# Optimization experiments

Measured on AMD Instinct MI355X. Metric: run time of the kernel, lower is better.

The kernel has to match this reference:

```python
import jax, jax.numpy as jnp
import numpy as np

B, NIMG, NTXT, EMB, INCH = 16, 1024, 512, 768, 768
EPS = 1e-5


def _bn(x, g, b):
    # train-mode BatchNorm1d over (batch, length) per channel; x: [B, L, C]
    mu = x.mean(axis=(0, 1))
    var = ((x - mu) ** 2).mean(axis=(0, 1))  # biased variance, as torch BN
    return g * (x - mu) * jax.lax.rsqrt(var + EPS) + b


def setup_inputs() -> dict:
    key = jax.random.key(0)
    ks = jax.random.split(key, 5)
    s = 1.0 / np.sqrt(EMB)
    return {
        "image": jax.random.normal(ks[0], (B, NIMG, INCH), jnp.float32),
        "text": jax.random.normal(ks[1], (B, NTXT, EMB), jnp.float32),
        "k": jax.random.uniform(ks[2], (B,), jnp.float32),
        "Wc": jax.random.normal(ks[3], (INCH, EMB), jnp.float32) * s,   # Conv1d k=1 weight
        "bc": jnp.zeros((INCH,), jnp.float32),
        "g1": jnp.ones((INCH,), jnp.float32),
        "b1": jnp.zeros((INCH,), jnp.float32),
        "Wout": jax.random.normal(ks[4], (INCH, EMB), jnp.float32) * s,  # Linear weight
        "bout": jnp.zeros((INCH,), jnp.float32),
        "g2": jnp.ones((INCH,), jnp.float32),
        "b2": jnp.zeros((INCH,), jnp.float32),
    }


def reference(image, text, k, Wc, bc, g1, b1, Wout, bout, g2, b2):
    Bn, N, C = image.shape
    T = text.shape[1]
    # emb1: Conv1d(1x1) -> BN -> ReLU, applied along tokens
    text_emb = jax.nn.relu(_bn(text @ Wc.T + bc, g1, b1))            # [B, T, C]
    attn = jnp.einsum('bnc,btc->bnt', image, text_emb) / np.sqrt(C)  # [B, N, T]
    # per-sample neighbor counts K_neigs = round(N * k)
    K_neigs = jnp.round(N * k).astype(jnp.int32)                     # [B]
    max_k = max(int(np.asarray(jnp.max(K_neigs))), 1)
    # top-k along the image-token axis (dim 1) => top_k on last axis of [B,T,N]
    attn_t = jnp.swapaxes(attn, 1, 2)                                # [B, T, N]
    _, idx = jax.lax.top_k(attn_t, max_k)                            # [B, T, max_k]
    valid = jnp.arange(max_k)[None, None, :] < K_neigs[:, None, None]
    valid = jnp.broadcast_to(valid, idx.shape)                       # [B, T, max_k]
    bi = jnp.arange(Bn)[:, None, None]
    ti = jnp.arange(T)[None, :, None]
    full_mask = jnp.zeros((Bn, T, N), bool).at[bi, ti, idx].set(valid)
    full_mask = jnp.swapaxes(full_mask, 1, 2)                        # [B, N, T]
    attn_sm = jax.nn.softmax(attn, axis=1)                           # softmax over N (dim=-2)
    v = text @ Wout.T + bout                                         # [B, T, C]
    out = jnp.einsum('bnt,btc->bnc', attn_sm * full_mask, v)         # [B, N, C]
    return jax.nn.relu(_bn(out, g2, b2)) + image
```

## Files before the change

kernel.cpp:

```cpp
#include <hip/hip_runtime.h>
#include <hip/hip_bf16.h>
#include <math.h>

typedef __attribute__((ext_vector_type(8))) short short8;
typedef __attribute__((ext_vector_type(4))) float f32x4;

static constexpr int kB  = 16;
static constexpr int kN  = 1024;
static constexpr int kT  = 512;
static constexpr int kC  = 768;
static constexpr float kEps = 1e-5f;

__device__ inline unsigned short f2bf(float x) {
    unsigned u = __float_as_uint(x);
    u += 0x7FFFu + ((u >> 16) & 1u);
    return (unsigned short)(u >> 16);
}
__device__ inline float bf2f(unsigned short h) {
    return __uint_as_float(((unsigned)h) << 16);
}

template<bool HAS_BIAS>
__global__ __launch_bounds__(256)
void gemm_sb(const unsigned short* __restrict__ A, const unsigned short* __restrict__ B,
             float* __restrict__ C, const float* __restrict__ bias,
             int N, int Kseg, float alpha, long sA, long sB, long sC)
{
    __shared__ unsigned short Ah[128 * 32];
    __shared__ unsigned short Al[128 * 32];
    __shared__ unsigned short Bh[128 * 32];
    __shared__ unsigned short Bl[128 * 32];
    const int bz = blockIdx.z;
    A += bz * sA;  B += bz * sB;  C += bz * sC;
    const int m0 = blockIdx.y * 128, n0 = blockIdx.x * 128;
    const int tid = threadIdx.x, lane = tid & 63, wid = tid >> 6;
    const int wm = wid & 1, wn = wid >> 1;
    const long ld = 2 * (long)Kseg;

    f32x4 acc[4][4] = {};

    const int srow  = lane >> 2;
    const int sslot = (lane & 3) ^ ((srow >> 1) & 3);
    const int r0    = wid * 32;
    const unsigned short* gA = A + (long)(m0 + r0 + srow) * ld + sslot * 8;
    const unsigned short* gB = B + (long)(n0 + r0 + srow) * ld + sslot * 8;

    const int frow  = lane & 15;
    const int fslot = (lane >> 4) ^ ((frow >> 1) & 3);

    for (int k0 = 0; k0 < Kseg; k0 += 32) {
        __syncthreads();
        {
            const unsigned short* ga = gA + k0;
            const unsigned short* gb = gB + k0;
#define GLDS(dst, src) __builtin_amdgcn_global_load_lds( \
            (const __attribute__((address_space(1))) void*)(src), \
            (__attribute__((address_space(3))) void*)(dst), 16, 0, 0)
            GLDS(Ah + r0 * 32,        ga);
            GLDS(Ah + (r0 + 16) * 32, ga + 16 * ld);
            GLDS(Al + r0 * 32,        ga + Kseg);
            GLDS(Al + (r0 + 16) * 32, ga + Kseg + 16 * ld);
            GLDS(Bh + r0 * 32,        gb);
            GLDS(Bh + (r0 + 16) * 32, gb + 16 * ld);
            GLDS(Bl + r0 * 32,        gb + Kseg);
            GLDS(Bl + (r0 + 16) * 32, gb + Kseg + 16 * ld);
#undef GLDS
        }
        __syncthreads();

        short8 ah[4], al[4], bh[4], bl[4];
#pragma unroll
        for (int f = 0; f < 4; ++f) {
            const int ra = (wm * 64 + f * 16 + frow) * 32 + fslot * 8;
            const int rb = (wn * 64 + f * 16 + frow) * 32 + fslot * 8;
            ah[f] = *(const short8*)(Ah + ra);
            al[f] = *(const short8*)(Al + ra);
            bh[f] = *(const short8*)(Bh + rb);
            bl[f] = *(const short8*)(Bl + rb);
        }
#pragma unroll
        for (int i = 0; i < 4; ++i)
#pragma unroll
            for (int j = 0; j < 4; ++j)
                acc[i][j] = __builtin_amdgcn_mfma_f32_16x16x32_bf16(
                    ah[i], bh[j], acc[i][j], 0, 0, 0);
#pragma unroll
        for (int i = 0; i < 4; ++i)
#pragma unroll
            for (int j = 0; j < 4; ++j)
                acc[i][j] = __builtin_amdgcn_mfma_f32_16x16x32_bf16(
                    al[i], bh[j], acc[i][j], 0, 0, 0);
#pragma unroll
        for (int i = 0; i < 4; ++i)
#pragma unroll
            for (int j = 0; j < 4; ++j)
                acc[i][j] = __builtin_amdgcn_mfma_f32_16x16x32_bf16(
                    ah[i], bl[j], acc[i][j], 0, 0, 0);
    }

    const int cn = lane & 15, rq = lane >> 4;
#pragma unroll
    for (int j = 0; j < 4; ++j) {
        const int n = n0 + wn * 64 + j * 16 + cn;
        const float bv = HAS_BIAS ? bias[n] : 0.f;
#pragma unroll
        for (int i = 0; i < 4; ++i) {
            const int mr = m0 + wm * 64 + i * 16 + rq * 4;
#pragma unroll
            for (int r = 0; r < 4; ++r)
                C[(long)(mr + r) * N + n] = acc[i][j][r] * alpha + bv;
        }
    }
}

__global__ void split2(const float* __restrict__ in, unsigned short* __restrict__ out,
                       int K, long total4)
{
    for (long i = blockIdx.x * (long)blockDim.x + threadIdx.x; i < total4;
         i += (long)gridDim.x * blockDim.x) {
        const long e = i * 4;
        const long row = e / K;
        const int  col = (int)(e - row * K);
        float4 x = *(const float4*)(in + e);
        ushort4 h, l;
        h.x = f2bf(x.x); l.x = f2bf(x.x - bf2f(h.x));
        h.y = f2bf(x.y); l.y = f2bf(x.y - bf2f(h.y));
        h.z = f2bf(x.z); l.z = f2bf(x.z - bf2f(h.z));
        h.w = f2bf(x.w); l.w = f2bf(x.w - bf2f(h.w));
        unsigned short* o = out + row * (long)(2 * K);
        *(ushort4*)(o + col)     = h;
        *(ushort4*)(o + K + col) = l;
    }
}

__global__ void split2_T(const float* __restrict__ in, unsigned short* __restrict__ out,
                         int R, int Cc, long sIn, long sOut)
{
    __shared__ float tile[32][33];
    const float* ib = in + (long)blockIdx.z * sIn;
    unsigned short* ob = out + (long)blockIdx.z * sOut;
    const int c0 = blockIdx.x * 32, r0 = blockIdx.y * 32;
    const int tx = threadIdx.x, ty = threadIdx.y;
#pragma unroll
    for (int it = 0; it < 4; ++it)
        tile[ty + 8 * it][tx] = ib[(long)(r0 + ty + 8 * it) * Cc + c0 + tx];
    __syncthreads();
#pragma unroll
    for (int it = 0; it < 4; ++it) {
        const int cc = ty + 8 * it;
        const float xv = tile[tx][cc];
        const unsigned short h = f2bf(xv);
        const unsigned short l = f2bf(xv - bf2f(h));
        unsigned short* o = ob + (long)(c0 + cc) * (2 * R) + r0 + tx;
        o[0] = h;  o[R] = l;
    }
}

__global__ void colstats(const float* __restrict__ X, float* __restrict__ sum,
                         float* __restrict__ sumsq, int rows_per_block)
{
    const int c  = threadIdx.x;
    const long r0 = (long)blockIdx.x * rows_per_block;
    float s0 = 0, s1 = 0, s2 = 0, q0 = 0, q1 = 0, q2 = 0;
    for (int r = 0; r < rows_per_block; ++r) {
        const float* row = X + (r0 + r) * kC;
        float x0 = row[c], x1 = row[c + 256], x2 = row[c + 512];
        s0 += x0; q0 += x0 * x0;
        s1 += x1; q1 += x1 * x1;
        s2 += x2; q2 += x2 * x2;
    }
    atomicAdd(&sum[c],       s0); atomicAdd(&sumsq[c],       q0);
    atomicAdd(&sum[c + 256], s1); atomicAdd(&sumsq[c + 256], q1);
    atomicAdd(&sum[c + 512], s2); atomicAdd(&sumsq[c + 512], q2);
}

__global__ void bn_relu_split2(const float* __restrict__ X, unsigned short* __restrict__ out,
                               const float* __restrict__ sum, const float* __restrict__ sumsq,
                               const float* __restrict__ g, const float* __restrict__ bta,
                               float invR, long total4)
{
    for (long i = blockIdx.x * (long)blockDim.x + threadIdx.x; i < total4;
         i += (long)gridDim.x * blockDim.x) {
        const long e = i * 4;
        const long row = e / kC;
        const int  c  = (int)(e - row * kC);
        float4 x = *(const float4*)(X + e);
        ushort4 h, l;
#pragma unroll
        for (int j = 0; j < 4; ++j) {
            const float mu  = sum[c + j] * invR;
            const float var = sumsq[c + j] * invR - mu * mu;
            float y = g[c + j] * ((&x.x)[j] - mu) * rsqrtf(var + kEps) + bta[c + j];
            y = fmaxf(y, 0.f);
            (&h.x)[j] = f2bf(y);
            (&l.x)[j] = f2bf(y - bf2f((&h.x)[j]));
        }
        unsigned short* o = out + row * (long)(2 * kC);
        *(ushort4*)(o + c)      = h;
        *(ushort4*)(o + kC + c) = l;
    }
}

__global__ void bn_relu_add(const float* __restrict__ X, const float* __restrict__ img,
                            float* __restrict__ out,
                            const float* __restrict__ sum, const float* __restrict__ sumsq,
                            const float* __restrict__ g, const float* __restrict__ bta,
                            float invR, long total4)
{
    for (long i = blockIdx.x * (long)blockDim.x + threadIdx.x; i < total4;
         i += (long)gridDim.x * blockDim.x) {
        float4 x  = ((const float4*)X)[i];
        float4 im = ((const float4*)img)[i];
        const int c = (int)((i * 4) % kC);
        float4 y;
#pragma unroll
        for (int j = 0; j < 4; ++j) {
            const float mu  = sum[c + j] * invR;
            const float var = sumsq[c + j] * invR - mu * mu;
            const float yy  = g[c + j] * ((&x.x)[j] - mu) * rsqrtf(var + kEps) + bta[c + j];
            (&y.x)[j] = fmaxf(yy, 0.f) + (&im.x)[j];
        }
        ((float4*)out)[i] = y;
    }
}

__global__ __launch_bounds__(256)
void topk_fused(float* __restrict__ attnT, const float* __restrict__ kfrac)
{
    __shared__ __align__(16) unsigned hist[256];
    __shared__ float redf[4];
    __shared__ unsigned sh_sel;
    __shared__ int sh_K;

    const int row  = blockIdx.x;
    const int b    = row >> 9;
    const int t    = threadIdx.x;
    const int lane = t & 63;
    const int wv   = t >> 6;
    float* x = attnT + (long)row * kN;

    float4 v = ((const float4*)x)[t];

    float m = fmaxf(fmaxf(v.x, v.y), fmaxf(v.z, v.w));
#pragma unroll
    for (int s = 32; s > 0; s >>= 1) m = fmaxf(m, __shfl_xor(m, s));
    if (lane == 0) redf[wv] = m;
    __syncthreads();
    const float M = fmaxf(fmaxf(redf[0], redf[1]), fmaxf(redf[2], redf[3]));
    __syncthreads();

    const float e0 = expf(v.x - M), e1 = expf(v.y - M);
    const float e2 = expf(v.z - M), e3 = expf(v.w - M);
    float e = (e0 + e1) + (e2 + e3);
#pragma unroll
    for (int s = 32; s > 0; s >>= 1) e += __shfl_xor(e, s);
    if (lane == 0) redf[wv] = e;
    __syncthreads();
    const float inv = 1.f / ((redf[0] + redf[1]) + (redf[2] + redf[3]));

    int K = (int)rintf((float)kN * kfrac[b]);
    float th;
    if (K <= 0) {
        th = __builtin_inff();
    } else if (K >= kN) {
        th = -__builtin_inff();
    } else {
        unsigned u[4];
#pragma unroll
        for (int j = 0; j < 4; ++j) {
            unsigned w = __float_as_uint((&v.x)[j]);
            u[j] = (w & 0x80000000u) ? ~w : (w | 0x80000000u);
        }
        unsigned prefix = 0, pm = 0;
        int Kr = K;
        for (int pos = 24; pos >= 0; pos -= 8) {
            hist[t] = 0;
            __syncthreads();
#pragma unroll
            for (int j = 0; j < 4; ++j)
                if ((u[j] & pm) == prefix)
                    atomicAdd(&hist[(u[j] >> pos) & 255u], 1u);
            __syncthreads();
            if (t < 64) {
                uint4 h = *(const uint4*)&hist[4 * t];
                unsigned s3 = h.w;
                unsigned s2 = h.z + s3;
                unsigned s1 = h.y + s2;
                unsigned s0 = h.x + s1;
                unsigned acc = s0;
#pragma unroll
                for (int s = 1; s < 64; s <<= 1) {
                    unsigned o = __shfl_down(acc, s);
                    if (lane + s < 64) acc += o;
                }
                const unsigned hiLanes = acc - s0;
                const unsigned g0 = s0 + hiLanes, g1 = s1 + hiLanes;
                const unsigned g2 = s2 + hiLanes, g3 = s3 + hiLanes;
                const unsigned kr = (unsigned)Kr;
                int dsel = -1; unsigned hex = 0;
                if      (g0 >= kr && g1 < kr)      { dsel = 4 * t + 0; hex = g1; }
                else if (g1 >= kr && g2 < kr)      { dsel = 4 * t + 1; hex = g2; }
                else if (g2 >= kr && g3 < kr)      { dsel = 4 * t + 2; hex = g3; }
                else if (g3 >= kr && hiLanes < kr) { dsel = 4 * t + 3; hex = hiLanes; }
                if (dsel >= 0) {
                    sh_sel = prefix | ((unsigned)dsel << pos);
                    sh_K   = (int)(kr - hex);
                }
            }
            __syncthreads();
            prefix = sh_sel;
            Kr     = sh_K;
            pm    |= (0xFFu << pos);
        }
        th = __uint_as_float((prefix & 0x80000000u) ? (prefix & 0x7FFFFFFFu) : ~prefix);
    }

    float4 y;
    y.x = (v.x >= th) ? e0 * inv : 0.f;
    y.y = (v.y >= th) ? e1 * inv : 0.f;
    y.z = (v.z >= th) ? e2 * inv : 0.f;
    y.w = (v.w >= th) ? e3 * inv : 0.f;
    ((float4*)x)[t] = y;
}

extern "C" void kernel_launch(void* const* d_in, const int* in_sizes, int n_in,
                              void* d_out, int out_size, void* d_ws, size_t ws_size,
                              hipStream_t stream)
{
    const float* image = (const float*)d_in[0];
    const float* text  = (const float*)d_in[1];
    const float* kfrac = (const float*)d_in[2];
    const float* Wc    = (const float*)d_in[3];
    const float* bc    = (const float*)d_in[4];
    const float* g1    = (const float*)d_in[5];
    const float* b1    = (const float*)d_in[6];
    const float* Wout  = (const float*)d_in[7];
    const float* bout  = (const float*)d_in[8];
    const float* g2    = (const float*)d_in[9];
    const float* b2    = (const float*)d_in[10];
    float* out = (float*)d_out;

    char* ws = (char*)d_ws;
    unsigned short* Wc2    = (unsigned short*)(ws + 0);
    unsigned short* Wout2  = (unsigned short*)(ws + 2359296);
    float*          stats  = (float*)(ws + 4718592);
    float*          v      = (float*)(ws + 4730880);
    float*          attnT  = (float*)(ws + 29896704);
    float*          temb   = (float*)(ws + 29896704);
    unsigned short* temb2  = (unsigned short*)(ws + 63451136);
    unsigned short* image2 = (unsigned short*)(ws + 88616960);
    unsigned short* text2  = (unsigned short*)(ws + 138948608);
    unsigned short* attn2T = (unsigned short*)(ws + 63451136);
    unsigned short* v2T    = (unsigned short*)(ws + 97005568);
    float*          outp   = (float*)(ws + 122171392);

    hipMemsetAsync(stats, 0, 4 * kC * sizeof(float), stream);

    const float inv_sqrt_c = 1.0f / sqrtf((float)kC);

    split2<<<dim3(1024), 256, 0, stream>>>(text,  text2,  kC, (long)kB * kT * kC / 4);
    split2<<<dim3(576),  256, 0, stream>>>(Wc,    Wc2,    kC, (long)kC * kC / 4);
    split2<<<dim3(576),  256, 0, stream>>>(Wout,  Wout2,  kC, (long)kC * kC / 4);
    split2<<<dim3(2048), 256, 0, stream>>>(image, image2, kC, (long)kB * kN * kC / 4);

    gemm_sb<true><<<dim3(kC / 128, (kB * kT) / 128, 1), 256, 0, stream>>>(
        text2, Wc2, temb, bc, kC, kC, 1.0f, 0, 0, 0);

    colstats<<<dim3((kB * kT) / 64), 256, 0, stream>>>(temb, stats, stats + kC, 64);
    bn_relu_split2<<<dim3(1024), 256, 0, stream>>>(temb, temb2, stats, stats + kC,
                                                   g1, b1, 1.0f / (kB * kT),
                                                   (long)kB * kT * kC / 4);

    gemm_sb<true><<<dim3(kC / 128, (kB * kT) / 128, 1), 256, 0, stream>>>(
        text2, Wout2, v, bout, kC, kC, 1.0f, 0, 0, 0);

    gemm_sb<false><<<dim3(kN / 128, kT / 128, kB), 256, 0, stream>>>(
        temb2, image2, attnT, nullptr, kN, kC, inv_sqrt_c,
        (long)kT * 2 * kC, (long)kN * 2 * kC, (long)kT * kN);

    topk_fused<<<dim3(kB * kT), 256, 0, stream>>>(attnT, kfrac);

    split2_T<<<dim3(kN / 32, kT / 32, kB), dim3(32, 8), 0, stream>>>(
        attnT, attn2T, kT, kN, (long)kT * kN, (long)kN * 2 * kT);
    split2_T<<<dim3(kC / 32, kT / 32, kB), dim3(32, 8), 0, stream>>>(
        v, v2T, kT, kC, (long)kT * kC, (long)kC * 2 * kT);

    gemm_sb<false><<<dim3(kC / 128, kN / 128, kB), 256, 0, stream>>>(
        attn2T, v2T, outp, nullptr, kC, kT, 1.0f,
        (long)kN * 2 * kT, (long)kC * 2 * kT, (long)kN * kC);

    colstats<<<dim3((kB * kN) / 64), 256, 0, stream>>>(outp, stats + 2 * kC,
                                                       stats + 3 * kC, 64);
    bn_relu_add<<<dim3(2048), 256, 0, stream>>>(outp, image, out,
                                                stats + 2 * kC, stats + 3 * kC,
                                                g2, b2, 1.0f / (kB * kN),
                                                (long)kB * kN * kC / 4);
}
```

Baseline: 474.1 us.

## Double-buffer GEMM LDS tiles and remap workgroups across XCDs

Turns the split-bf16 GEMM main loop into a two-stage LDS pipeline. The next K-tile is prefetched with global_load_lds while the current tile is consumed, using explicit vmcnt waits and raw barriers. It also launches a flat 1D grid and remaps block IDs so consecutive tiles land on the same XCD, which should improve L2 reuse. Doubling shared memory to 64KB may lower occupancy, and the hand-written waitcnt/barrier ordering is fragile.

```diff
diff --git a/kernel.cpp b/kernel.cpp
--- a/kernel.cpp
+++ b/kernel.cpp
@@ -24,15 +24,22 @@
 __global__ __launch_bounds__(256)
 void gemm_sb(const unsigned short* __restrict__ A, const unsigned short* __restrict__ B,
              float* __restrict__ C, const float* __restrict__ bias,
-             int N, int Kseg, float alpha, long sA, long sB, long sC)
-{
-    __shared__ unsigned short Ah[128 * 32];
-    __shared__ unsigned short Al[128 * 32];
-    __shared__ unsigned short Bh[128 * 32];
-    __shared__ unsigned short Bl[128 * 32];
-    const int bz = blockIdx.z;
-    A += bz * sA;  B += bz * sB;  C += bz * sC;
-    const int m0 = blockIdx.y * 128, n0 = blockIdx.x * 128;
+             int N, int Kseg, float alpha, long sA, long sB, long sC,
+             int gx, int gy)
+{
+    __shared__ unsigned short Ah[2][128 * 32];
+    __shared__ unsigned short Al[2][128 * 32];
+    __shared__ unsigned short Bh[2][128 * 32];
+    __shared__ unsigned short Bl[2][128 * 32];
+
+    const unsigned nwg = gridDim.x;
+    unsigned g = (blockIdx.x & 7u) * (nwg >> 3) + (blockIdx.x >> 3);
+    const int bxx = (int)(g % (unsigned)gx);  g /= (unsigned)gx;
+    const int byy = (int)(g % (unsigned)gy);
+    const int bz  = (int)(g / (unsigned)gy);
+
+    A += (long)bz * sA;  B += (long)bz * sB;  C += (long)bz * sC;
+    const int m0 = byy * 128, n0 = bxx * 128;
     const int tid = threadIdx.x, lane = tid & 63, wid = tid >> 6;
     const int wm = wid & 1, wn = wid >> 1;
     const long ld = 2 * (long)Kseg;
@@ -48,35 +55,45 @@
     const int frow  = lane & 15;
     const int fslot = (lane >> 4) ^ ((frow >> 1) & 3);
 
-    for (int k0 = 0; k0 < Kseg; k0 += 32) {
-        __syncthreads();
-        {
-            const unsigned short* ga = gA + k0;
-            const unsigned short* gb = gB + k0;
+    const int NK = Kseg / 32;
+
 #define GLDS(dst, src) __builtin_amdgcn_global_load_lds( \
-            (const __attribute__((address_space(1))) void*)(src), \
-            (__attribute__((address_space(3))) void*)(dst), 16, 0, 0)
-            GLDS(Ah + r0 * 32,        ga);
-            GLDS(Ah + (r0 + 16) * 32, ga + 16 * ld);
-            GLDS(Al + r0 * 32,        ga + Kseg);
-            GLDS(Al + (r0 + 16) * 32, ga + Kseg + 16 * ld);
-            GLDS(Bh + r0 * 32,        gb);
-            GLDS(Bh + (r0 + 16) * 32, gb + 16 * ld);
-            GLDS(Bl + r0 * 32,        gb + Kseg);
-            GLDS(Bl + (r0 + 16) * 32, gb + Kseg + 16 * ld);
+        (const __attribute__((address_space(1))) void*)(src), \
+        (__attribute__((address_space(3))) void*)(dst), 16, 0, 0)
+    auto stage = [&](int ks, int p) {
+        const unsigned short* ga = gA + ks * 32;
+        const unsigned short* gb = gB + ks * 32;
+        GLDS(&Ah[p][r0 * 32],        ga);
+        GLDS(&Ah[p][(r0 + 16) * 32], ga + 16 * ld);
+        GLDS(&Al[p][r0 * 32],        ga + Kseg);
+        GLDS(&Al[p][(r0 + 16) * 32], ga + Kseg + 16 * ld);
+        GLDS(&Bh[p][r0 * 32],        gb);
+        GLDS(&Bh[p][(r0 + 16) * 32], gb + 16 * ld);
+        GLDS(&Bl[p][r0 * 32],        gb + Kseg);
+        GLDS(&Bl[p][(r0 + 16) * 32], gb + Kseg + 16 * ld);
+    };
 #undef GLDS
-        }
-        __syncthreads();
+
+    stage(0, 0);
+    for (int ks = 0; ks < NK; ++ks) {
+        const int p = ks & 1;
+        if (ks + 1 < NK) {
+            stage(ks + 1, p ^ 1);
+            asm volatile("s_waitcnt vmcnt(8)" ::: "memory");
+        } else {
+            asm volatile("s_waitcnt vmcnt(0)" ::: "memory");
+        }
+        __builtin_amdgcn_s_barrier();
 
         short8 ah[4], al[4], bh[4], bl[4];
 #pragma unroll
         for (int f = 0; f < 4; ++f) {
             const int ra = (wm * 64 + f * 16 + frow) * 32 + fslot * 8;
             const int rb = (wn * 64 + f * 16 + frow) * 32 + fslot * 8;
-            ah[f] = *(const short8*)(Ah + ra);
-            al[f] = *(const short8*)(Al + ra);
-            bh[f] = *(const short8*)(Bh + rb);
-            bl[f] = *(const short8*)(Bl + rb);
+            ah[f] = *(const short8*)(&Ah[p][ra]);
+            al[f] = *(const short8*)(&Al[p][ra]);
+            bh[f] = *(const short8*)(&Bh[p][rb]);
+            bl[f] = *(const short8*)(&Bl[p][rb]);
         }
 #pragma unroll
         for (int i = 0; i < 4; ++i)
@@ -96,6 +113,8 @@
             for (int j = 0; j < 4; ++j)
                 acc[i][j] = __builtin_amdgcn_mfma_f32_16x16x32_bf16(
                     ah[i], bl[j], acc[i][j], 0, 0, 0);
+
+        __builtin_amdgcn_s_barrier();
     }
 
     const int cn = lane & 15, rq = lane >> 4;
@@ -363,20 +382,20 @@
     split2<<<dim3(576),  256, 0, stream>>>(Wout,  Wout2,  kC, (long)kC * kC / 4);
     split2<<<dim3(2048), 256, 0, stream>>>(image, image2, kC, (long)kB * kN * kC / 4);
 
-    gemm_sb<true><<<dim3(kC / 128, (kB * kT) / 128, 1), 256, 0, stream>>>(
-        text2, Wc2, temb, bc, kC, kC, 1.0f, 0, 0, 0);
+    gemm_sb<true><<<384, 256, 0, stream>>>(
+        text2, Wc2, temb, bc, kC, kC, 1.0f, 0, 0, 0, 6, 64);
 
     colstats<<<dim3((kB * kT) / 64), 256, 0, stream>>>(temb, stats, stats + kC, 64);
     bn_relu_split2<<<dim3(1024), 256, 0, stream>>>(temb, temb2, stats, stats + kC,
                                                    g1, b1, 1.0f / (kB * kT),
                                                    (long)kB * kT * kC / 4);
 
-    gemm_sb<true><<<dim3(kC / 128, (kB * kT) / 128, 1), 256, 0, stream>>>(
-        text2, Wout2, v, bout, kC, kC, 1.0f, 0, 0, 0);
-
-    gemm_sb<false><<<dim3(kN / 128, kT / 128, kB), 256, 0, stream>>>(
+    gemm_sb<true><<<384, 256, 0, stream>>>(
+        text2, Wout2, v, bout, kC, kC, 1.0f, 0, 0, 0, 6, 64);
+
+    gemm_sb<false><<<512, 256, 0, stream>>>(
         temb2, image2, attnT, nullptr, kN, kC, inv_sqrt_c,
-        (long)kT * 2 * kC, (long)kN * 2 * kC, (long)kT * kN);
+        (long)kT * 2 * kC, (long)kN * 2 * kC, (long)kT * kN, 8, 4);
 
     topk_fused<<<dim3(kB * kT), 256, 0, stream>>>(attnT, kfrac);
 
@@ -385,9 +404,9 @@
     split2_T<<<dim3(kC / 32, kT / 32, kB), dim3(32, 8), 0, stream>>>(
         v, v2T, kT, kC, (long)kT * kC, (long)kC * 2 * kT);
 
-    gemm_sb<false><<<dim3(kC / 128, kN / 128, kB), 256, 0, stream>>>(
+    gemm_sb<false><<<768, 256, 0, stream>>>(
         attn2T, v2T, outp, nullptr, kC, kT, 1.0f,
-        (long)kN * 2 * kT, (long)kC * 2 * kT, (long)kN * kC);
+        (long)kN * 2 * kT, (long)kC * 2 * kT, (long)kN * kC, 6, 8);
 
     colstats<<<dim3((kB * kN) / 64), 256, 0, stream>>>(outp, stats + 2 * kC,
                                                        stats + 3 * kC, 64);
```

Measured after the change: 422.4 us. -10.9%, faster.
